# Performance work log

Measured on AMD Instinct MI355X. Metric: run time of the kernel, lower is better.

The kernel has to match this reference:

```python
import jax, jax.numpy as jnp
import numpy as np

H = 16  # num_heads (from init_kwargs)


def setup_inputs() -> dict:
    key = jax.random.key(0)
    ks = jax.random.split(key, 12)
    B, S, E = 4, 1024, 1024
    inp = {
        "query": jax.random.normal(ks[0], (B, S, E), jnp.float32),
        "key": jax.random.normal(ks[1], (B, S, E), jnp.float32),
        "value": jax.random.normal(ks[2], (B, S, E), jnp.float32),
        "mask": jax.random.randint(ks[3], (B, S, S), 0, 2, jnp.int32),
        # nn.Linear params: y = x @ W.T + b
        "Wq": jax.random.normal(ks[4], (E, E), jnp.float32) * 0.02,
        "bq": jnp.zeros((E,), jnp.float32),
        "Wk": jax.random.normal(ks[5], (E, E), jnp.float32) * 0.02,
        "bk": jnp.zeros((E,), jnp.float32),
        "Wv": jax.random.normal(ks[6], (E, E), jnp.float32) * 0.02,
        "bv": jnp.zeros((E,), jnp.float32),
        "Wo": jax.random.normal(ks[7], (E, E), jnp.float32) * 0.02,
        "bo": jnp.zeros((E,), jnp.float32),
    }
    return inp


def reference(query, key, value, mask, Wq, bq, Wk, bk, Wv, bv, Wo, bo):
    # Dropout treated as identity (eval mode) for a deterministic baseline.
    B, Sq, E = query.shape
    Sk = key.shape[1]
    D = E // H
    scale = jnp.sqrt(jnp.float32(D))

    Q = (query @ Wq.T + bq).reshape(B, Sq, H, D).transpose(0, 2, 1, 3)  # bhqd
    K = (key @ Wk.T + bk).reshape(B, Sk, H, D).transpose(0, 2, 1, 3)    # bhkd
    V = (value @ Wv.T + bv).reshape(B, Sk, H, D).transpose(0, 2, 1, 3)  # bhkd

    scores = jnp.einsum("bhqd,bhkd->bhqk", Q, K) / scale
    scores = jnp.where(mask[:, None, :, :] == 0, jnp.float32(-1e9), scores)
    attn = jax.nn.softmax(scores, axis=-1)  # [B,H,Sq,Sk]

    ctx = jnp.einsum("bhqk,bhkd->bhqd", attn, V)
    ctx = ctx.transpose(0, 2, 1, 3).reshape(B, Sq, E)
    out = ctx @ Wo.T + bo
    attn_avg = attn.mean(axis=1)  # [B,Sq,Sk]
    return out, attn_avg
```

## Files before the change

kernel.cpp:

```cpp
#include <hip/hip_runtime.h>
#include <hip/hip_bf16.h>
#include <stdint.h>

#define BATCH 4
#define SEQ   1024
#define EMB   1024
#define NH    16
#define HD    64

typedef short s8v __attribute__((ext_vector_type(8)));
typedef float f4v __attribute__((ext_vector_type(4)));

__device__ __forceinline__ uint16_t f2bf(float f) {
    __hip_bfloat16 h = __float2bfloat16(f);
    return *reinterpret_cast<uint16_t*>(&h);
}
__device__ __forceinline__ short bfraw(float f) {
    __hip_bfloat16 h = __float2bfloat16(f);
    return *reinterpret_cast<short*>(&h);
}
__device__ __forceinline__ s8v cvt8(const float* p) {
    float4 a = *(const float4*)p;
    float4 b = *(const float4*)(p + 4);
    s8v r;
    r[0] = bfraw(a.x); r[1] = bfraw(a.y); r[2] = bfraw(a.z); r[3] = bfraw(a.w);
    r[4] = bfraw(b.x); r[5] = bfraw(b.y); r[6] = bfraw(b.z); r[7] = bfraw(b.w);
    return r;
}

__global__ __launch_bounds__(256) void pack_mask(
        const int* __restrict__ mask, unsigned long long* __restrict__ Mb64)
{
    const size_t gid = (size_t)blockIdx.x * 256 + threadIdx.x;
    const unsigned long long bal = __ballot(mask[gid] != 0);
    if ((threadIdx.x & 63) == 0) Mb64[gid >> 6] = bal;
}

__global__ __launch_bounds__(256) void cvt_all(
        const float* __restrict__ W0, const float* __restrict__ W1,
        const float* __restrict__ W2, const float* __restrict__ W3,
        const float* __restrict__ X0, const float* __restrict__ X1,
        const float* __restrict__ X2,
        uint16_t* __restrict__ Wdst, uint16_t* __restrict__ Xq,
        uint16_t* __restrict__ Xk, uint16_t* __restrict__ Xv)
{
    const int y = blockIdx.y;
    const size_t off = ((size_t)blockIdx.x * 256 + threadIdx.x) * 8;
    if (y < 4) {
        if (blockIdx.x >= 512) return;
        const float* s = (y == 0) ? W0 : (y == 1) ? W1 : (y == 2) ? W2 : W3;
        *(s8v*)(Wdst + (size_t)y * EMB * EMB + off) = cvt8(s + off);
    } else {
        const float* s = (y == 4) ? X0 : (y == 5) ? X1 : X2;
        uint16_t*    d = (y == 4) ? Xq : (y == 5) ? Xk : Xv;
        *(s8v*)(d + off) = cvt8(s + off);
    }
}

__global__ __launch_bounds__(512, 2) void proj_gemm(
        const uint16_t* __restrict__ Xb, const uint16_t* __restrict__ Wb,
        const float* __restrict__ bias, void* __restrict__ outv,
        int scatter, float scale)
{
    __shared__ __attribute__((aligned(16))) uint16_t As[128][32];
    __shared__ __attribute__((aligned(16))) uint16_t Bs[128][32];

    const int t    = threadIdx.x;
    const int lane = t & 63;
    const int w    = t >> 6;
    const int wm = w & 1;
    const int wn = w >> 1;
    const int m0 = blockIdx.y * 128;
    const int n0 = blockIdx.x * 128;
    const int ar = lane & 15;
    const int aq = lane >> 4;

    const int srow = t >> 2;
    const int scol = (t & 3) * 8;

    const uint16_t* gA = Xb + (size_t)(m0 + srow) * EMB + scol;
    const uint16_t* gB = Wb + (size_t)(n0 + srow) * EMB + scol;

    f4v acc[4][2];
    #pragma unroll
    for (int i = 0; i < 4; ++i)
        #pragma unroll
        for (int j = 0; j < 2; ++j) acc[i][j] = (f4v){0.f, 0.f, 0.f, 0.f};

    s8v ra = *(const s8v*)gA;
    s8v rb = *(const s8v*)gB;

    for (int k0 = 0; k0 < EMB; k0 += 32) {
        __syncthreads();
        *(s8v*)&As[srow][scol] = ra;
        *(s8v*)&Bs[srow][scol] = rb;
        const int kn = (k0 + 32) & (EMB - 1);
        ra = *(const s8v*)(gA + kn);
        rb = *(const s8v*)(gB + kn);
        __syncthreads();

        s8v af[4], bf[2];
        #pragma unroll
        for (int i = 0; i < 4; ++i)
            af[i] = *(const s8v*)&As[wm * 64 + i * 16 + ar][aq * 8];
        #pragma unroll
        for (int j = 0; j < 2; ++j)
            bf[j] = *(const s8v*)&Bs[wn * 32 + j * 16 + ar][aq * 8];
        #pragma unroll
        for (int i = 0; i < 4; ++i)
            #pragma unroll
            for (int j = 0; j < 2; ++j)
                acc[i][j] = __builtin_amdgcn_mfma_f32_16x16x32_bf16(af[i], bf[j], acc[i][j], 0, 0, 0);
    }

    #pragma unroll
    for (int i = 0; i < 4; ++i) {
        const int crow = m0 + wm * 64 + i * 16 + aq * 4;
        #pragma unroll
        for (int j = 0; j < 2; ++j) {
            const int n = n0 + wn * 32 + j * 16 + ar;
            const float bv = bias[n];
            #pragma unroll
            for (int r = 0; r < 4; ++r) {
                const int m = crow + r;
                const float v = (acc[i][j][r] + bv) * scale;
                if (scatter == 1) {
                    size_t idx = (size_t)(((m >> 10) * NH + (n >> 6)) * SEQ + (m & 1023)) * HD + (n & 63);
                    ((uint16_t*)outv)[idx] = f2bf(v);
                } else if (scatter == 2) {
                    size_t idx = (size_t)(((m >> 10) * NH + (n >> 6)) * HD + (n & 63)) * SEQ + (m & 1023);
                    ((uint16_t*)outv)[idx] = f2bf(v);
                } else {
                    ((float*)outv)[(size_t)m * EMB + n] = v;
                }
            }
        }
    }
}

__global__ __launch_bounds__(256, 4) void flash_ctx(
        const uint16_t* __restrict__ Qb, const uint16_t* __restrict__ Kb,
        const uint16_t* __restrict__ Vt, const uint32_t* __restrict__ Mb,
        uint16_t* __restrict__ ctx, float* __restrict__ linv_out)
{
    __shared__ uint32_t Ml[4][16][33];
    __shared__ __attribute__((aligned(16))) uint16_t Pt[4][2][16][56];

    const int t = threadIdx.x;
    const int w = t >> 6, lane = t & 63;
    const int ar = lane & 15, aq = lane >> 4;

    const int id   = blockIdx.x;
    const int xcd  = id & 7;
    const int rest = id >> 3;
    const int bh   = xcd * 8 + (rest & 7);
    const int qt   = (rest >> 3) * 4 + w;
    const int b = bh >> 4, h = bh & 15;
    const size_t hb = ((size_t)(b * NH + h)) * SEQ * HD;

    {
        const uint32_t* src = Mb + (((size_t)b * SEQ + qt * 16) << 5);
        uint4 m0 = *(const uint4*)(src + lane * 8);
        uint4 m1 = *(const uint4*)(src + lane * 8 + 4);
        const int pr = (lane * 8) >> 5, pc = (lane * 8) & 31;
        Ml[w][pr][pc + 0] = m0.x; Ml[w][pr][pc + 1] = m0.y;
        Ml[w][pr][pc + 2] = m0.z; Ml[w][pr][pc + 3] = m0.w;
        Ml[w][pr][pc + 4] = m1.x; Ml[w][pr][pc + 5] = m1.y;
        Ml[w][pr][pc + 6] = m1.z; Ml[w][pr][pc + 7] = m1.w;
    }

    const uint16_t* qp = Qb + hb + (size_t)(qt * 16 + ar) * HD + aq * 8;
    const s8v a0 = *(const s8v*)qp;
    const s8v a1 = *(const s8v*)(qp + 32);

    const uint16_t* kbase = Kb + hb + (size_t)ar * HD + aq * 8;
    const uint16_t* vbase = Vt + hb + (size_t)ar * SEQ + aq * 8;

    f4v O0 = {0.f,0.f,0.f,0.f}, O1 = O0, O2 = O0, O3 = O0;
    float lsum[4] = {0.f, 0.f, 0.f, 0.f};

    s8v cbl0 = *(const s8v*)kbase;
    s8v cbh0 = *(const s8v*)(kbase + 32);
    s8v cbl1 = *(const s8v*)(kbase + 16 * HD);
    s8v cbh1 = *(const s8v*)(kbase + 16 * HD + 32);
    s8v cvv0 = *(const s8v*)vbase;
    s8v cvv1 = *(const s8v*)(vbase + 16 * SEQ);
    s8v cvv2 = *(const s8v*)(vbase + 32 * SEQ);
    s8v cvv3 = *(const s8v*)(vbase + 48 * SEQ);

    #pragma unroll 2
    for (int ci = 0; ci < 32; ++ci) {
        f4v z = {0.f,0.f,0.f,0.f};
        f4v s0 = __builtin_amdgcn_mfma_f32_16x16x32_bf16(a0, cbl0, z, 0, 0, 0);
        s0 = __builtin_amdgcn_mfma_f32_16x16x32_bf16(a1, cbh0, s0, 0, 0, 0);
        f4v s1 = __builtin_amdgcn_mfma_f32_16x16x32_bf16(a0, cbl1, z, 0, 0, 0);
        s1 = __builtin_amdgcn_mfma_f32_16x16x32_bf16(a1, cbh1, s1, 0, 0, 0);

        const int kcn = ((ci + 1) & 31) * 32;
        const uint16_t* kn = kbase + (size_t)kcn * HD;
        const uint16_t* vn = vbase + kcn;
        s8v nbl0 = *(const s8v*)kn;
        s8v nbh0 = *(const s8v*)(kn + 32);
        s8v nbl1 = *(const s8v*)(kn + 16 * HD);
        s8v nbh1 = *(const s8v*)(kn + 16 * HD + 32);
        s8v nvv0 = *(const s8v*)vn;
        s8v nvv1 = *(const s8v*)(vn + 16 * SEQ);
        s8v nvv2 = *(const s8v*)(vn + 32 * SEQ);
        s8v nvv3 = *(const s8v*)(vn + 48 * SEQ);

        const int pb = ci & 1;
        #pragma unroll
        for (int r = 0; r < 4; ++r) {
            const uint32_t mw = Ml[w][aq * 4 + r][ci];
            const float e0 = ((mw >> ar) & 1u)        ? __expf(s0[r]) : 0.f;
            const float e1 = ((mw >> (16 + ar)) & 1u) ? __expf(s1[r]) : 0.f;
            lsum[r] += e0 + e1;
            Pt[w][pb][aq * 4 + r][ar]      = f2bf(e0);
            Pt[w][pb][aq * 4 + r][16 + ar] = f2bf(e1);
        }

        const s8v pa = *(const s8v*)&Pt[w][pb][ar][aq * 8];
        O0 = __builtin_amdgcn_mfma_f32_16x16x32_bf16(pa, cvv0, O0, 0, 0, 0);
        O1 = __builtin_amdgcn_mfma_f32_16x16x32_bf16(pa, cvv1, O1, 0, 0, 0);
        O2 = __builtin_amdgcn_mfma_f32_16x16x32_bf16(pa, cvv2, O2, 0, 0, 0);
        O3 = __builtin_amdgcn_mfma_f32_16x16x32_bf16(pa, cvv3, O3, 0, 0, 0);

        cbl0 = nbl0; cbh0 = nbh0; cbl1 = nbl1; cbh1 = nbh1;
        cvv0 = nvv0; cvv1 = nvv1; cvv2 = nvv2; cvv3 = nvv3;
    }

    #pragma unroll
    for (int off = 1; off < 16; off <<= 1) {
        #pragma unroll
        for (int r = 0; r < 4; ++r) lsum[r] += __shfl_xor(lsum[r], off);
    }
    float inv[4];
    #pragma unroll
    for (int r = 0; r < 4; ++r) inv[r] = 1.0f / lsum[r];

    #pragma unroll
    for (int r = 0; r < 4; ++r) {
        const int q = qt * 16 + aq * 4 + r;
        uint16_t* cp = ctx + ((size_t)(b * SEQ + q) * NH + h) * HD + ar;
        cp[ 0] = f2bf(O0[r] * inv[r]);
        cp[16] = f2bf(O1[r] * inv[r]);
        cp[32] = f2bf(O2[r] * inv[r]);
        cp[48] = f2bf(O3[r] * inv[r]);
    }
    if (ar == 0) {
        #pragma unroll
        for (int r = 0; r < 4; ++r)
            linv_out[(size_t)(b * NH + h) * SEQ + qt * 16 + aq * 4 + r] = inv[r];
    }
}

__global__ __launch_bounds__(512, 2) void attn_avg(
        const uint16_t* __restrict__ Qb, const uint16_t* __restrict__ Kb,
        const uint32_t* __restrict__ Mb, const float* __restrict__ linv,
        float* __restrict__ attn_out)
{
    const int qt = blockIdx.x;
    const int b  = blockIdx.y >> 1;
    const int kh = blockIdx.y & 1;
    const int t = threadIdx.x;
    const int w = t >> 6, lane = t & 63;
    const int ar = lane & 15, aq = lane >> 4;
    const int k0 = kh * 512 + w * 64;

    uint32_t mw0[4], mw1[4];
    #pragma unroll
    for (int r = 0; r < 4; ++r) {
        const uint32_t* mp = Mb + (((size_t)b * SEQ + qt * 16 + aq * 4 + r) << 5) + (k0 >> 5);
        mw0[r] = mp[0]; mw1[r] = mp[1];
    }

    float acc[16];
    #pragma unroll
    for (int j = 0; j < 16; ++j) acc[j] = 0.f;

    for (int h = 0; h < NH; ++h) {
        const size_t hb = ((size_t)(b * NH + h)) * SEQ * HD;
        const uint16_t* qp = Qb + hb + (size_t)(qt * 16 + ar) * HD + aq * 8;
        const s8v a0 = *(const s8v*)qp;
        const s8v a1 = *(const s8v*)(qp + 32);
        float fs[4];
        #pragma unroll
        for (int r = 0; r < 4; ++r)
            fs[r] = linv[(size_t)(b * NH + h) * SEQ + qt * 16 + aq * 4 + r] * 0.0625f;

        #pragma unroll
        for (int nt = 0; nt < 4; ++nt) {
            const uint16_t* kp = Kb + hb + (size_t)(k0 + nt * 16 + ar) * HD + aq * 8;
            s8v bl = *(const s8v*)kp, bh2 = *(const s8v*)(kp + 32);
            f4v z = {0.f,0.f,0.f,0.f};
            f4v s = __builtin_amdgcn_mfma_f32_16x16x32_bf16(a0, bl, z, 0, 0, 0);
            s = __builtin_amdgcn_mfma_f32_16x16x32_bf16(a1, bh2, s, 0, 0, 0);
            #pragma unroll
            for (int r = 0; r < 4; ++r) {
                const uint32_t mword = (nt & 2) ? mw1[r] : mw0[r];
                const int bit = ((nt & 1) << 4) + ar;
                if ((mword >> bit) & 1u) acc[r * 4 + nt] += __expf(s[r]) * fs[r];
            }
        }
    }

    #pragma unroll
    for (int r = 0; r < 4; ++r) {
        float* ap = attn_out + ((size_t)b * SEQ + qt * 16 + aq * 4 + r) * SEQ + k0 + ar;
        #pragma unroll
        for (int nt = 0; nt < 4; ++nt) ap[nt * 16] = acc[r * 4 + nt];
    }
}

extern "C" void kernel_launch(void* const* d_in, const int* in_sizes, int n_in,
                              void* d_out, int out_size, void* d_ws, size_t ws_size,
                              hipStream_t stream) {
    const float* q_in = (const float*)d_in[0];
    const float* k_in = (const float*)d_in[1];
    const float* v_in = (const float*)d_in[2];
    const int*   mask = (const int*)d_in[3];
    const float* Wq = (const float*)d_in[4];
    const float* bq = (const float*)d_in[5];
    const float* Wk = (const float*)d_in[6];
    const float* bk = (const float*)d_in[7];
    const float* Wv = (const float*)d_in[8];
    const float* bv = (const float*)d_in[9];
    const float* Wo = (const float*)d_in[10];
    const float* bo = (const float*)d_in[11];

    float* out      = (float*)d_out;
    float* attn_out = out + (size_t)BATCH * SEQ * EMB;

    const size_t qkv_elems = (size_t)BATCH * NH * SEQ * HD;
    uint16_t* Qb  = (uint16_t*)d_ws;
    uint16_t* Kb  = Qb + qkv_elems;
    uint16_t* Vt  = Kb + qkv_elems;
    uint16_t* ctx = Vt + qkv_elems;
    uint16_t* Wcb = ctx + (size_t)BATCH * SEQ * EMB;
    uint16_t* Wqb = Wcb;
    uint16_t* Wkb = Wcb + (size_t)EMB * EMB;
    uint16_t* Wvb = Wcb + 2 * (size_t)EMB * EMB;
    uint16_t* Wob = Wcb + 3 * (size_t)EMB * EMB;
    uint16_t* Xq  = Wcb + 4 * (size_t)EMB * EMB;
    uint16_t* Xk  = Xq + qkv_elems;
    uint16_t* Xv  = ctx;
    uint32_t* Mb32 = (uint32_t*)(Xk + qkv_elems);
    float*    linv = (float*)(Mb32 + (size_t)BATCH * SEQ * 32);

    pack_mask<<<dim3((BATCH * SEQ * SEQ) / 256), 256, 0, stream>>>(
        mask, (unsigned long long*)Mb32);
    cvt_all<<<dim3(2048, 7), 256, 0, stream>>>(Wq, Wk, Wv, Wo, q_in, k_in, v_in,
                                               Wcb, Xq, Xk, Xv);

    dim3 ggrid(EMB / 128, (BATCH * SEQ) / 128);
    proj_gemm<<<ggrid, 512, 0, stream>>>(Xq, Wqb, bq, Qb, 1, 0.125f);
    proj_gemm<<<ggrid, 512, 0, stream>>>(Xk, Wkb, bk, Kb, 1, 1.0f);
    proj_gemm<<<ggrid, 512, 0, stream>>>(Xv, Wvb, bv, Vt, 2, 1.0f);

    flash_ctx<<<dim3(1024), 256, 0, stream>>>(Qb, Kb, Vt, Mb32, ctx, linv);
    attn_avg<<<dim3(SEQ / 16, BATCH * 2), 512, 0, stream>>>(Qb, Kb, Mb32, linv, attn_out);

    proj_gemm<<<ggrid, 512, 0, stream>>>(ctx, Wob, bo, out, 0, 1.0f);
}
```

Measured before the change: 411.8 us.

## Batch QKV GEMMs into one launch, split flash keys across warps, shrink tiles

The three projection GEMMs become a single launch that picks Q, K or V by blockIdx.z, and the GEMM tile drops from 128x128 with 512 threads to 64x64 with 256 threads. The flash attention kernel now splits the key range between two warp pairs and merges their partial O and row sums through shared memory, which doubles the grid. It also drops the register prefetch of the next K/V chunk. attn_avg is split into four key quarters for more blocks. The aim is fewer launches and more parallelism and occupancy, at the cost of less data reuse per tile, an extra reduction step, and less latency hiding in the flash loop.

```diff
diff --git a/kernel.cpp b/kernel.cpp
--- a/kernel.cpp
+++ b/kernel.cpp
@@ -57,21 +57,32 @@
     }
 }
 
-__global__ __launch_bounds__(512, 2) void proj_gemm(
-        const uint16_t* __restrict__ Xb, const uint16_t* __restrict__ Wb,
-        const float* __restrict__ bias, void* __restrict__ outv,
-        int scatter, float scale)
-{
-    __shared__ __attribute__((aligned(16))) uint16_t As[128][32];
-    __shared__ __attribute__((aligned(16))) uint16_t Bs[128][32];
+__global__ __launch_bounds__(256, 4) void gemm3(
+        const uint16_t* __restrict__ X0, const uint16_t* __restrict__ W0,
+        const float* __restrict__ b0, void* __restrict__ o0, int sc0, float ss0,
+        const uint16_t* __restrict__ X1, const uint16_t* __restrict__ W1,
+        const float* __restrict__ b1, void* __restrict__ o1, int sc1, float ss1,
+        const uint16_t* __restrict__ X2, const uint16_t* __restrict__ W2,
+        const float* __restrict__ b2, void* __restrict__ o2, int sc2, float ss2)
+{
+    __shared__ __attribute__((aligned(16))) uint16_t As[64][40];
+    __shared__ __attribute__((aligned(16))) uint16_t Bs[64][40];
+
+    const int z = blockIdx.z;
+    const uint16_t* Xb   = (z == 0) ? X0 : (z == 1) ? X1 : X2;
+    const uint16_t* Wb   = (z == 0) ? W0 : (z == 1) ? W1 : W2;
+    const float*    bias = (z == 0) ? b0 : (z == 1) ? b1 : b2;
+    void*           outv = (z == 0) ? o0 : (z == 1) ? o1 : o2;
+    const int     scatter = (z == 0) ? sc0 : (z == 1) ? sc1 : sc2;
+    const float   scale   = (z == 0) ? ss0 : (z == 1) ? ss1 : ss2;
 
     const int t    = threadIdx.x;
     const int lane = t & 63;
     const int w    = t >> 6;
     const int wm = w & 1;
     const int wn = w >> 1;
-    const int m0 = blockIdx.y * 128;
-    const int n0 = blockIdx.x * 128;
+    const int m0 = blockIdx.y * 64;
+    const int n0 = blockIdx.x * 64;
     const int ar = lane & 15;
     const int aq = lane >> 4;
 
@@ -81,9 +92,9 @@
     const uint16_t* gA = Xb + (size_t)(m0 + srow) * EMB + scol;
     const uint16_t* gB = Wb + (size_t)(n0 + srow) * EMB + scol;
 
-    f4v acc[4][2];
-    #pragma unroll
-    for (int i = 0; i < 4; ++i)
+    f4v acc[2][2];
+    #pragma unroll
+    for (int i = 0; i < 2; ++i)
         #pragma unroll
         for (int j = 0; j < 2; ++j) acc[i][j] = (f4v){0.f, 0.f, 0.f, 0.f};
 
@@ -99,23 +110,23 @@
         rb = *(const s8v*)(gB + kn);
         __syncthreads();
 
-        s8v af[4], bf[2];
-        #pragma unroll
-        for (int i = 0; i < 4; ++i)
-            af[i] = *(const s8v*)&As[wm * 64 + i * 16 + ar][aq * 8];
+        s8v af[2], bf[2];
+        #pragma unroll
+        for (int i = 0; i < 2; ++i)
+            af[i] = *(const s8v*)&As[wm * 32 + i * 16 + ar][aq * 8];
         #pragma unroll
         for (int j = 0; j < 2; ++j)
             bf[j] = *(const s8v*)&Bs[wn * 32 + j * 16 + ar][aq * 8];
         #pragma unroll
-        for (int i = 0; i < 4; ++i)
+        for (int i = 0; i < 2; ++i)
             #pragma unroll
             for (int j = 0; j < 2; ++j)
                 acc[i][j] = __builtin_amdgcn_mfma_f32_16x16x32_bf16(af[i], bf[j], acc[i][j], 0, 0, 0);
     }
 
     #pragma unroll
-    for (int i = 0; i < 4; ++i) {
-        const int crow = m0 + wm * 64 + i * 16 + aq * 4;
+    for (int i = 0; i < 2; ++i) {
+        const int crow = m0 + wm * 32 + i * 16 + aq * 4;
         #pragma unroll
         for (int j = 0; j < 2; ++j) {
             const int n = n0 + wn * 32 + j * 16 + ar;
@@ -138,36 +149,40 @@
     }
 }
 
-__global__ __launch_bounds__(256, 4) void flash_ctx(
+__global__ __launch_bounds__(256, 8) void flash_ctx(
         const uint16_t* __restrict__ Qb, const uint16_t* __restrict__ Kb,
         const uint16_t* __restrict__ Vt, const uint32_t* __restrict__ Mb,
         uint16_t* __restrict__ ctx, float* __restrict__ linv_out)
 {
-    __shared__ uint32_t Ml[4][16][33];
-    __shared__ __attribute__((aligned(16))) uint16_t Pt[4][2][16][56];
+    __shared__ uint32_t Ml[2][16][33];
+    __shared__ __attribute__((aligned(16))) char shbuf[14336];
+    auto Pt = reinterpret_cast<uint16_t(*)[2][16][56]>(shbuf);
+    auto Oc = reinterpret_cast<float(*)[64][21]>(shbuf);
 
     const int t = threadIdx.x;
     const int w = t >> 6, lane = t & 63;
     const int ar = lane & 15, aq = lane >> 4;
-
-    const int id   = blockIdx.x;
-    const int xcd  = id & 7;
-    const int rest = id >> 3;
-    const int bh   = xcd * 8 + (rest & 7);
-    const int qt   = (rest >> 3) * 4 + w;
+    const int qt_local = w & 1, khalf = w >> 1;
+
+    const int id    = blockIdx.x;
+    const int xcd   = id & 7;
+    const int rest  = id >> 3;
+    const int bh    = xcd * 8 + (rest & 7);
+    const int qpair = rest >> 3;
+    const int qt    = qpair * 2 + qt_local;
     const int b = bh >> 4, h = bh & 15;
     const size_t hb = ((size_t)(b * NH + h)) * SEQ * HD;
 
     {
-        const uint32_t* src = Mb + (((size_t)b * SEQ + qt * 16) << 5);
-        uint4 m0 = *(const uint4*)(src + lane * 8);
-        uint4 m1 = *(const uint4*)(src + lane * 8 + 4);
-        const int pr = (lane * 8) >> 5, pc = (lane * 8) & 31;
-        Ml[w][pr][pc + 0] = m0.x; Ml[w][pr][pc + 1] = m0.y;
-        Ml[w][pr][pc + 2] = m0.z; Ml[w][pr][pc + 3] = m0.w;
-        Ml[w][pr][pc + 4] = m1.x; Ml[w][pr][pc + 5] = m1.y;
-        Ml[w][pr][pc + 6] = m1.z; Ml[w][pr][pc + 7] = m1.w;
-    }
+        const uint32_t* src = Mb + (((size_t)b * SEQ + qpair * 32) << 5);
+        uint4 m = *(const uint4*)(src + t * 4);
+        const int row = t >> 3, col = (t & 7) * 4;
+        Ml[row >> 4][row & 15][col + 0] = m.x;
+        Ml[row >> 4][row & 15][col + 1] = m.y;
+        Ml[row >> 4][row & 15][col + 2] = m.z;
+        Ml[row >> 4][row & 15][col + 3] = m.w;
+    }
+    __syncthreads();
 
     const uint16_t* qp = Qb + hb + (size_t)(qt * 16 + ar) * HD + aq * 8;
     const s8v a0 = *(const s8v*)qp;
@@ -179,39 +194,24 @@
     f4v O0 = {0.f,0.f,0.f,0.f}, O1 = O0, O2 = O0, O3 = O0;
     float lsum[4] = {0.f, 0.f, 0.f, 0.f};
 
-    s8v cbl0 = *(const s8v*)kbase;
-    s8v cbh0 = *(const s8v*)(kbase + 32);
-    s8v cbl1 = *(const s8v*)(kbase + 16 * HD);
-    s8v cbh1 = *(const s8v*)(kbase + 16 * HD + 32);
-    s8v cvv0 = *(const s8v*)vbase;
-    s8v cvv1 = *(const s8v*)(vbase + 16 * SEQ);
-    s8v cvv2 = *(const s8v*)(vbase + 32 * SEQ);
-    s8v cvv3 = *(const s8v*)(vbase + 48 * SEQ);
-
     #pragma unroll 2
-    for (int ci = 0; ci < 32; ++ci) {
+    for (int ci = 0; ci < 16; ++ci) {
+        const int c  = khalf * 16 + ci;
+        const int kc = c * 32;
+        const uint16_t* k0 = kbase + (size_t)kc * HD;
+        const uint16_t* k1 = k0 + 16 * HD;
+        s8v bl0 = *(const s8v*)k0, bh0 = *(const s8v*)(k0 + 32);
+        s8v bl1 = *(const s8v*)k1, bh1 = *(const s8v*)(k1 + 32);
         f4v z = {0.f,0.f,0.f,0.f};
-        f4v s0 = __builtin_amdgcn_mfma_f32_16x16x32_bf16(a0, cbl0, z, 0, 0, 0);
-        s0 = __builtin_amdgcn_mfma_f32_16x16x32_bf16(a1, cbh0, s0, 0, 0, 0);
-        f4v s1 = __builtin_amdgcn_mfma_f32_16x16x32_bf16(a0, cbl1, z, 0, 0, 0);
-        s1 = __builtin_amdgcn_mfma_f32_16x16x32_bf16(a1, cbh1, s1, 0, 0, 0);
-
-        const int kcn = ((ci + 1) & 31) * 32;
-        const uint16_t* kn = kbase + (size_t)kcn * HD;
-        const uint16_t* vn = vbase + kcn;
-        s8v nbl0 = *(const s8v*)kn;
-        s8v nbh0 = *(const s8v*)(kn + 32);
-        s8v nbl1 = *(const s8v*)(kn + 16 * HD);
-        s8v nbh1 = *(const s8v*)(kn + 16 * HD + 32);
-        s8v nvv0 = *(const s8v*)vn;
-        s8v nvv1 = *(const s8v*)(vn + 16 * SEQ);
-        s8v nvv2 = *(const s8v*)(vn + 32 * SEQ);
-        s8v nvv3 = *(const s8v*)(vn + 48 * SEQ);
+        f4v s0 = __builtin_amdgcn_mfma_f32_16x16x32_bf16(a0, bl0, z, 0, 0, 0);
+        s0 = __builtin_amdgcn_mfma_f32_16x16x32_bf16(a1, bh0, s0, 0, 0, 0);
+        f4v s1 = __builtin_amdgcn_mfma_f32_16x16x32_bf16(a0, bl1, z, 0, 0, 0);
+        s1 = __builtin_amdgcn_mfma_f32_16x16x32_bf16(a1, bh1, s1, 0, 0, 0);
 
         const int pb = ci & 1;
         #pragma unroll
         for (int r = 0; r < 4; ++r) {
-            const uint32_t mw = Ml[w][aq * 4 + r][ci];
+            const uint32_t mw = Ml[qt_local][aq * 4 + r][c];
             const float e0 = ((mw >> ar) & 1u)        ? __expf(s0[r]) : 0.f;
             const float e1 = ((mw >> (16 + ar)) & 1u) ? __expf(s1[r]) : 0.f;
             lsum[r] += e0 + e1;
@@ -220,13 +220,15 @@
         }
 
         const s8v pa = *(const s8v*)&Pt[w][pb][ar][aq * 8];
-        O0 = __builtin_amdgcn_mfma_f32_16x16x32_bf16(pa, cvv0, O0, 0, 0, 0);
-        O1 = __builtin_amdgcn_mfma_f32_16x16x32_bf16(pa, cvv1, O1, 0, 0, 0);
-        O2 = __builtin_amdgcn_mfma_f32_16x16x32_bf16(pa, cvv2, O2, 0, 0, 0);
-        O3 = __builtin_amdgcn_mfma_f32_16x16x32_bf16(pa, cvv3, O3, 0, 0, 0);
-
-        cbl0 = nbl0; cbh0 = nbh0; cbl1 = nbl1; cbh1 = nbh1;
-        cvv0 = nvv0; cvv1 = nvv1; cvv2 = nvv2; cvv3 = nvv3;
+        const uint16_t* v0 = vbase + kc;
+        s8v vv0 = *(const s8v*)(v0);
+        s8v vv1 = *(const s8v*)(v0 + 16 * SEQ);
+        s8v vv2 = *(const s8v*)(v0 + 32 * SEQ);
+        s8v vv3 = *(const s8v*)(v0 + 48 * SEQ);
+        O0 = __builtin_amdgcn_mfma_f32_16x16x32_bf16(pa, vv0, O0, 0, 0, 0);
+        O1 = __builtin_amdgcn_mfma_f32_16x16x32_bf16(pa, vv1, O1, 0, 0, 0);
+        O2 = __builtin_amdgcn_mfma_f32_16x16x32_bf16(pa, vv2, O2, 0, 0, 0);
+        O3 = __builtin_amdgcn_mfma_f32_16x16x32_bf16(pa, vv3, O3, 0, 0, 0);
     }
 
     #pragma unroll
@@ -234,49 +236,68 @@
         #pragma unroll
         for (int r = 0; r < 4; ++r) lsum[r] += __shfl_xor(lsum[r], off);
     }
-    float inv[4];
-    #pragma unroll
-    for (int r = 0; r < 4; ++r) inv[r] = 1.0f / lsum[r];
-
-    #pragma unroll
-    for (int r = 0; r < 4; ++r) {
-        const int q = qt * 16 + aq * 4 + r;
-        uint16_t* cp = ctx + ((size_t)(b * SEQ + q) * NH + h) * HD + ar;
-        cp[ 0] = f2bf(O0[r] * inv[r]);
-        cp[16] = f2bf(O1[r] * inv[r]);
-        cp[32] = f2bf(O2[r] * inv[r]);
-        cp[48] = f2bf(O3[r] * inv[r]);
-    }
-    if (ar == 0) {
-        #pragma unroll
-        for (int r = 0; r < 4; ++r)
-            linv_out[(size_t)(b * NH + h) * SEQ + qt * 16 + aq * 4 + r] = inv[r];
-    }
-}
-
-__global__ __launch_bounds__(512, 2) void attn_avg(
+
+    __syncthreads();
+    if (khalf == 1) {
+        float* d = Oc[qt_local][lane];
+        #pragma unroll
+        for (int r = 0; r < 4; ++r) {
+            d[r]      = O0[r];  d[4 + r]  = O1[r];
+            d[8 + r]  = O2[r];  d[12 + r] = O3[r];
+            d[16 + r] = lsum[r];
+        }
+    }
+    __syncthreads();
+    if (khalf == 0) {
+        const float* s = Oc[qt_local][lane];
+        #pragma unroll
+        for (int r = 0; r < 4; ++r) {
+            O0[r] += s[r];      O1[r] += s[4 + r];
+            O2[r] += s[8 + r];  O3[r] += s[12 + r];
+            lsum[r] += s[16 + r];
+        }
+        float inv[4];
+        #pragma unroll
+        for (int r = 0; r < 4; ++r) inv[r] = 1.0f / lsum[r];
+
+        #pragma unroll
+        for (int r = 0; r < 4; ++r) {
+            const int q = qt * 16 + aq * 4 + r;
+            uint16_t* cp = ctx + ((size_t)(b * SEQ + q) * NH + h) * HD + ar;
+            cp[ 0] = f2bf(O0[r] * inv[r]);
+            cp[16] = f2bf(O1[r] * inv[r]);
+            cp[32] = f2bf(O2[r] * inv[r]);
+            cp[48] = f2bf(O3[r] * inv[r]);
+        }
+        if (ar == 0) {
+            #pragma unroll
+            for (int r = 0; r < 4; ++r)
+                linv_out[(size_t)(b * NH + h) * SEQ + qt * 16 + aq * 4 + r] = inv[r];
+        }
+    }
+}
+
+__global__ __launch_bounds__(512, 8) void attn_avg(
         const uint16_t* __restrict__ Qb, const uint16_t* __restrict__ Kb,
         const uint32_t* __restrict__ Mb, const float* __restrict__ linv,
         float* __restrict__ attn_out)
 {
     const int qt = blockIdx.x;
-    const int b  = blockIdx.y >> 1;
-    const int kh = blockIdx.y & 1;
+    const int b  = blockIdx.y >> 2;
+    const int kq = blockIdx.y & 3;
     const int t = threadIdx.x;
     const int w = t >> 6, lane = t & 63;
     const int ar = lane & 15, aq = lane >> 4;
-    const int k0 = kh * 512 + w * 64;
-
-    uint32_t mw0[4], mw1[4];
-    #pragma unroll
-    for (int r = 0; r < 4; ++r) {
-        const uint32_t* mp = Mb + (((size_t)b * SEQ + qt * 16 + aq * 4 + r) << 5) + (k0 >> 5);
-        mw0[r] = mp[0]; mw1[r] = mp[1];
-    }
-
-    float acc[16];
-    #pragma unroll
-    for (int j = 0; j < 16; ++j) acc[j] = 0.f;
+    const int k0 = kq * 256 + w * 32;
+
+    uint32_t mw[4];
+    #pragma unroll
+    for (int r = 0; r < 4; ++r)
+        mw[r] = Mb[(((size_t)b * SEQ + qt * 16 + aq * 4 + r) << 5) + (k0 >> 5)];
+
+    float acc[8];
+    #pragma unroll
+    for (int j = 0; j < 8; ++j) acc[j] = 0.f;
 
     for (int h = 0; h < NH; ++h) {
         const size_t hb = ((size_t)(b * NH + h)) * SEQ * HD;
@@ -289,7 +310,7 @@
             fs[r] = linv[(size_t)(b * NH + h) * SEQ + qt * 16 + aq * 4 + r] * 0.0625f;
 
         #pragma unroll
-        for (int nt = 0; nt < 4; ++nt) {
+        for (int nt = 0; nt < 2; ++nt) {
             const uint16_t* kp = Kb + hb + (size_t)(k0 + nt * 16 + ar) * HD + aq * 8;
             s8v bl = *(const s8v*)kp, bh2 = *(const s8v*)(kp + 32);
             f4v z = {0.f,0.f,0.f,0.f};
@@ -297,9 +318,8 @@
             s = __builtin_amdgcn_mfma_f32_16x16x32_bf16(a1, bh2, s, 0, 0, 0);
             #pragma unroll
             for (int r = 0; r < 4; ++r) {
-                const uint32_t mword = (nt & 2) ? mw1[r] : mw0[r];
-                const int bit = ((nt & 1) << 4) + ar;
-                if ((mword >> bit) & 1u) acc[r * 4 + nt] += __expf(s[r]) * fs[r];
+                const int bit = nt * 16 + ar;
+                if ((mw[r] >> bit) & 1u) acc[r * 2 + nt] += __expf(s[r]) * fs[r];
             }
         }
     }
@@ -308,7 +328,7 @@
     for (int r = 0; r < 4; ++r) {
         float* ap = attn_out + ((size_t)b * SEQ + qt * 16 + aq * 4 + r) * SEQ + k0 + ar;
         #pragma unroll
-        for (int nt = 0; nt < 4; ++nt) ap[nt * 16] = acc[r * 4 + nt];
+        for (int nt = 0; nt < 2; ++nt) ap[nt * 16] = acc[r * 2 + nt];
     }
 }
 
@@ -352,13 +372,18 @@
     cvt_all<<<dim3(2048, 7), 256, 0, stream>>>(Wq, Wk, Wv, Wo, q_in, k_in, v_in,
                                                Wcb, Xq, Xk, Xv);
 
-    dim3 ggrid(EMB / 128, (BATCH * SEQ) / 128);
-    proj_gemm<<<ggrid, 512, 0, stream>>>(Xq, Wqb, bq, Qb, 1, 0.125f);
-    proj_gemm<<<ggrid, 512, 0, stream>>>(Xk, Wkb, bk, Kb, 1, 1.0f);
-    proj_gemm<<<ggrid, 512, 0, stream>>>(Xv, Wvb, bv, Vt, 2, 1.0f);
-
-    flash_ctx<<<dim3(1024), 256, 0, stream>>>(Qb, Kb, Vt, Mb32, ctx, linv);
-    attn_avg<<<dim3(SEQ / 16, BATCH * 2), 512, 0, stream>>>(Qb, Kb, Mb32, linv, attn_out);
-
-    proj_gemm<<<ggrid, 512, 0, stream>>>(ctx, Wob, bo, out, 0, 1.0f);
-}
+    dim3 g3(EMB / 64, (BATCH * SEQ) / 64, 3);
+    gemm3<<<g3, 256, 0, stream>>>(
+        Xq, Wqb, bq, Qb, 1, 0.125f,
+        Xk, Wkb, bk, Kb, 1, 1.0f,
+        Xv, Wvb, bv, Vt, 2, 1.0f);
+
+    flash_ctx<<<dim3(2048), 256, 0, stream>>>(Qb, Kb, Vt, Mb32, ctx, linv);
+    attn_avg<<<dim3(SEQ / 16, BATCH * 4), 512, 0, stream>>>(Qb, Kb, Mb32, linv, attn_out);
+
+    dim3 g1(EMB / 64, (BATCH * SEQ) / 64, 1);
+    gemm3<<<g1, 256, 0, stream>>>(
+        ctx, Wob, bo, out, 0, 1.0f,
+        ctx, Wob, bo, out, 0, 1.0f,
+        ctx, Wob, bo, out, 0, 1.0f);
+}
```

Result: slower. 516.8 us (+25.5%).

## Batch QKV GEMMs, pad LDS tiles, dual-stream flash loop, split attn_avg finer

Applied to the files above, without the earlier changes.

The three Q/K/V projection GEMMs become one launch with blockIdx.z selecting the operands, and the LDS tiles get a row pad from 32 to 40 elements to cut bank conflicts. The flash_ctx loop now handles two key chunks per iteration with separate accumulators instead of software-prefetching the next chunk, which aims for more MFMA independence but needs more registers. attn_avg splits keys into quarters instead of halves with launch bounds of 4 blocks, doubling the block count and reducing per-thread state.

```diff
diff --git a/kernel.cpp b/kernel.cpp
--- a/kernel.cpp
+++ b/kernel.cpp
@@ -57,13 +57,24 @@
     }
 }
 
-__global__ __launch_bounds__(512, 2) void proj_gemm(
-        const uint16_t* __restrict__ Xb, const uint16_t* __restrict__ Wb,
-        const float* __restrict__ bias, void* __restrict__ outv,
-        int scatter, float scale)
+__global__ __launch_bounds__(512, 2) void gemm3(
+        const uint16_t* __restrict__ X0, const uint16_t* __restrict__ W0,
+        const float* __restrict__ b0, void* __restrict__ o0, int sc0, float ss0,
+        const uint16_t* __restrict__ X1, const uint16_t* __restrict__ W1,
+        const float* __restrict__ b1, void* __restrict__ o1, int sc1, float ss1,
+        const uint16_t* __restrict__ X2, const uint16_t* __restrict__ W2,
+        const float* __restrict__ b2, void* __restrict__ o2, int sc2, float ss2)
 {
-    __shared__ __attribute__((aligned(16))) uint16_t As[128][32];
-    __shared__ __attribute__((aligned(16))) uint16_t Bs[128][32];
+    __shared__ __attribute__((aligned(16))) uint16_t As[128][40];
+    __shared__ __attribute__((aligned(16))) uint16_t Bs[128][40];
+
+    const int z = blockIdx.z;
+    const uint16_t* Xb   = (z == 0) ? X0 : (z == 1) ? X1 : X2;
+    const uint16_t* Wb   = (z == 0) ? W0 : (z == 1) ? W1 : W2;
+    const float*    bias = (z == 0) ? b0 : (z == 1) ? b1 : b2;
+    void*           outv = (z == 0) ? o0 : (z == 1) ? o1 : o2;
+    const int     scatter = (z == 0) ? sc0 : (z == 1) ? sc1 : sc2;
+    const float   scale   = (z == 0) ? ss0 : (z == 1) ? ss1 : ss2;
 
     const int t    = threadIdx.x;
     const int lane = t & 63;
@@ -176,57 +187,80 @@
     const uint16_t* kbase = Kb + hb + (size_t)ar * HD + aq * 8;
     const uint16_t* vbase = Vt + hb + (size_t)ar * SEQ + aq * 8;
 
-    f4v O0 = {0.f,0.f,0.f,0.f}, O1 = O0, O2 = O0, O3 = O0;
-    float lsum[4] = {0.f, 0.f, 0.f, 0.f};
-
-    s8v cbl0 = *(const s8v*)kbase;
-    s8v cbh0 = *(const s8v*)(kbase + 32);
-    s8v cbl1 = *(const s8v*)(kbase + 16 * HD);
-    s8v cbh1 = *(const s8v*)(kbase + 16 * HD + 32);
-    s8v cvv0 = *(const s8v*)vbase;
-    s8v cvv1 = *(const s8v*)(vbase + 16 * SEQ);
-    s8v cvv2 = *(const s8v*)(vbase + 32 * SEQ);
-    s8v cvv3 = *(const s8v*)(vbase + 48 * SEQ);
-
-    #pragma unroll 2
-    for (int ci = 0; ci < 32; ++ci) {
+    f4v OA0 = {0.f,0.f,0.f,0.f}, OA1 = OA0, OA2 = OA0, OA3 = OA0;
+    f4v OB0 = OA0, OB1 = OA0, OB2 = OA0, OB3 = OA0;
+    float lsA[4] = {0.f, 0.f, 0.f, 0.f};
+    float lsB[4] = {0.f, 0.f, 0.f, 0.f};
+
+    for (int ci = 0; ci < 16; ++ci) {
+        const int cA = ci * 2, cB = ci * 2 + 1;
+        const int kcA = cA * 32, kcB = cB * 32;
+
+        const uint16_t* kA = kbase + (size_t)kcA * HD;
+        const uint16_t* kB = kbase + (size_t)kcB * HD;
+        s8v Abl0 = *(const s8v*)kA,            Abh0 = *(const s8v*)(kA + 32);
+        s8v Abl1 = *(const s8v*)(kA + 16*HD),  Abh1 = *(const s8v*)(kA + 16*HD + 32);
+        s8v Bbl0 = *(const s8v*)kB,            Bbh0 = *(const s8v*)(kB + 32);
+        s8v Bbl1 = *(const s8v*)(kB + 16*HD),  Bbh1 = *(const s8v*)(kB + 16*HD + 32);
+
         f4v z = {0.f,0.f,0.f,0.f};
-        f4v s0 = __builtin_amdgcn_mfma_f32_16x16x32_bf16(a0, cbl0, z, 0, 0, 0);
-        s0 = __builtin_amdgcn_mfma_f32_16x16x32_bf16(a1, cbh0, s0, 0, 0, 0);
-        f4v s1 = __builtin_amdgcn_mfma_f32_16x16x32_bf16(a0, cbl1, z, 0, 0, 0);
-        s1 = __builtin_amdgcn_mfma_f32_16x16x32_bf16(a1, cbh1, s1, 0, 0, 0);
-
-        const int kcn = ((ci + 1) & 31) * 32;
-        const uint16_t* kn = kbase + (size_t)kcn * HD;
-        const uint16_t* vn = vbase + kcn;
-        s8v nbl0 = *(const s8v*)kn;
-        s8v nbh0 = *(const s8v*)(kn + 32);
-        s8v nbl1 = *(const s8v*)(kn + 16 * HD);
-        s8v nbh1 = *(const s8v*)(kn + 16 * HD + 32);
-        s8v nvv0 = *(const s8v*)vn;
-        s8v nvv1 = *(const s8v*)(vn + 16 * SEQ);
-        s8v nvv2 = *(const s8v*)(vn + 32 * SEQ);
-        s8v nvv3 = *(const s8v*)(vn + 48 * SEQ);
-
-        const int pb = ci & 1;
+        f4v sA0 = __builtin_amdgcn_mfma_f32_16x16x32_bf16(a0, Abl0, z, 0, 0, 0);
+        sA0 = __builtin_amdgcn_mfma_f32_16x16x32_bf16(a1, Abh0, sA0, 0, 0, 0);
+        f4v sA1 = __builtin_amdgcn_mfma_f32_16x16x32_bf16(a0, Abl1, z, 0, 0, 0);
+        sA1 = __builtin_amdgcn_mfma_f32_16x16x32_bf16(a1, Abh1, sA1, 0, 0, 0);
+        f4v sB0 = __builtin_amdgcn_mfma_f32_16x16x32_bf16(a0, Bbl0, z, 0, 0, 0);
+        sB0 = __builtin_amdgcn_mfma_f32_16x16x32_bf16(a1, Bbh0, sB0, 0, 0, 0);
+        f4v sB1 = __builtin_amdgcn_mfma_f32_16x16x32_bf16(a0, Bbl1, z, 0, 0, 0);
+        sB1 = __builtin_amdgcn_mfma_f32_16x16x32_bf16(a1, Bbh1, sB1, 0, 0, 0);
+
+        const uint16_t* vA = vbase + kcA;
+        const uint16_t* vB = vbase + kcB;
+        s8v Av0 = *(const s8v*)(vA);
+        s8v Av1 = *(const s8v*)(vA + 16 * SEQ);
+        s8v Av2 = *(const s8v*)(vA + 32 * SEQ);
+        s8v Av3 = *(const s8v*)(vA + 48 * SEQ);
+        s8v Bv0 = *(const s8v*)(vB);
+        s8v Bv1 = *(const s8v*)(vB + 16 * SEQ);
+        s8v Bv2 = *(const s8v*)(vB + 32 * SEQ);
+        s8v Bv3 = *(const s8v*)(vB + 48 * SEQ);
+
         #pragma unroll
         for (int r = 0; r < 4; ++r) {
-            const uint32_t mw = Ml[w][aq * 4 + r][ci];
-            const float e0 = ((mw >> ar) & 1u)        ? __expf(s0[r]) : 0.f;
-            const float e1 = ((mw >> (16 + ar)) & 1u) ? __expf(s1[r]) : 0.f;
-            lsum[r] += e0 + e1;
-            Pt[w][pb][aq * 4 + r][ar]      = f2bf(e0);
-            Pt[w][pb][aq * 4 + r][16 + ar] = f2bf(e1);
+            const uint32_t mwA = Ml[w][aq * 4 + r][cA];
+            const float e0 = ((mwA >> ar) & 1u)        ? __expf(sA0[r]) : 0.f;
+            const float e1 = ((mwA >> (16 + ar)) & 1u) ? __expf(sA1[r]) : 0.f;
+            lsA[r] += e0 + e1;
+            Pt[w][0][aq * 4 + r][ar]      = f2bf(e0);
+            Pt[w][0][aq * 4 + r][16 + ar] = f2bf(e1);
         }
-
-        const s8v pa = *(const s8v*)&Pt[w][pb][ar][aq * 8];
-        O0 = __builtin_amdgcn_mfma_f32_16x16x32_bf16(pa, cvv0, O0, 0, 0, 0);
-        O1 = __builtin_amdgcn_mfma_f32_16x16x32_bf16(pa, cvv1, O1, 0, 0, 0);
-        O2 = __builtin_amdgcn_mfma_f32_16x16x32_bf16(pa, cvv2, O2, 0, 0, 0);
-        O3 = __builtin_amdgcn_mfma_f32_16x16x32_bf16(pa, cvv3, O3, 0, 0, 0);
-
-        cbl0 = nbl0; cbh0 = nbh0; cbl1 = nbl1; cbh1 = nbh1;
-        cvv0 = nvv0; cvv1 = nvv1; cvv2 = nvv2; cvv3 = nvv3;
+        #pragma unroll
+        for (int r = 0; r < 4; ++r) {
+            const uint32_t mwB = Ml[w][aq * 4 + r][cB];
+            const float e0 = ((mwB >> ar) & 1u)        ? __expf(sB0[r]) : 0.f;
+            const float e1 = ((mwB >> (16 + ar)) & 1u) ? __expf(sB1[r]) : 0.f;
+            lsB[r] += e0 + e1;
+            Pt[w][1][aq * 4 + r][ar]      = f2bf(e0);
+            Pt[w][1][aq * 4 + r][16 + ar] = f2bf(e1);
+        }
+
+        const s8v paA = *(const s8v*)&Pt[w][0][ar][aq * 8];
+        OA0 = __builtin_amdgcn_mfma_f32_16x16x32_bf16(paA, Av0, OA0, 0, 0, 0);
+        OA1 = __builtin_amdgcn_mfma_f32_16x16x32_bf16(paA, Av1, OA1, 0, 0, 0);
+        OA2 = __builtin_amdgcn_mfma_f32_16x16x32_bf16(paA, Av2, OA2, 0, 0, 0);
+        OA3 = __builtin_amdgcn_mfma_f32_16x16x32_bf16(paA, Av3, OA3, 0, 0, 0);
+        const s8v paB = *(const s8v*)&Pt[w][1][ar][aq * 8];
+        OB0 = __builtin_amdgcn_mfma_f32_16x16x32_bf16(paB, Bv0, OB0, 0, 0, 0);
+        OB1 = __builtin_amdgcn_mfma_f32_16x16x32_bf16(paB, Bv1, OB1, 0, 0, 0);
+        OB2 = __builtin_amdgcn_mfma_f32_16x16x32_bf16(paB, Bv2, OB2, 0, 0, 0);
+        OB3 = __builtin_amdgcn_mfma_f32_16x16x32_bf16(paB, Bv3, OB3, 0, 0, 0);
+    }
+
+    float lsum[4];
+    #pragma unroll
+    for (int r = 0; r < 4; ++r) {
+        OA0[r] += OB0[r]; OA1[r] += OB1[r];
+        OA2[r] += OB2[r]; OA3[r] += OB3[r];
+        lsum[r] = lsA[r] + lsB[r];
     }
 
     #pragma unroll
@@ -242,10 +276,10 @@
     for (int r = 0; r < 4; ++r) {
         const int q = qt * 16 + aq * 4 + r;
         uint16_t* cp = ctx + ((size_t)(b * SEQ + q) * NH + h) * HD + ar;
-        cp[ 0] = f2bf(O0[r] * inv[r]);
-        cp[16] = f2bf(O1[r] * inv[r]);
-        cp[32] = f2bf(O2[r] * inv[r]);
-        cp[48] = f2bf(O3[r] * inv[r]);
+        cp[ 0] = f2bf(OA0[r] * inv[r]);
+        cp[16] = f2bf(OA1[r] * inv[r]);
+        cp[32] = f2bf(OA2[r] * inv[r]);
+        cp[48] = f2bf(OA3[r] * inv[r]);
     }
     if (ar == 0) {
         #pragma unroll
@@ -254,29 +288,27 @@
     }
 }
 
-__global__ __launch_bounds__(512, 2) void attn_avg(
+__global__ __launch_bounds__(512, 4) void attn_avg(
         const uint16_t* __restrict__ Qb, const uint16_t* __restrict__ Kb,
         const uint32_t* __restrict__ Mb, const float* __restrict__ linv,
         float* __restrict__ attn_out)
 {
     const int qt = blockIdx.x;
-    const int b  = blockIdx.y >> 1;
-    const int kh = blockIdx.y & 1;
+    const int b  = blockIdx.y >> 2;
+    const int kq = blockIdx.y & 3;
     const int t = threadIdx.x;
     const int w = t >> 6, lane = t & 63;
     const int ar = lane & 15, aq = lane >> 4;
-    const int k0 = kh * 512 + w * 64;
-
-    uint32_t mw0[4], mw1[4];
-    #pragma unroll
-    for (int r = 0; r < 4; ++r) {
-        const uint32_t* mp = Mb + (((size_t)b * SEQ + qt * 16 + aq * 4 + r) << 5) + (k0 >> 5);
-        mw0[r] = mp[0]; mw1[r] = mp[1];
-    }
-
-    float acc[16];
-    #pragma unroll
-    for (int j = 0; j < 16; ++j) acc[j] = 0.f;
+    const int k0 = kq * 256 + w * 32;
+
+    uint32_t mw[4];
+    #pragma unroll
+    for (int r = 0; r < 4; ++r)
+        mw[r] = Mb[(((size_t)b * SEQ + qt * 16 + aq * 4 + r) << 5) + (k0 >> 5)];
+
+    float acc[8];
+    #pragma unroll
+    for (int j = 0; j < 8; ++j) acc[j] = 0.f;
 
     for (int h = 0; h < NH; ++h) {
         const size_t hb = ((size_t)(b * NH + h)) * SEQ * HD;
@@ -289,7 +321,7 @@
             fs[r] = linv[(size_t)(b * NH + h) * SEQ + qt * 16 + aq * 4 + r] * 0.0625f;
 
         #pragma unroll
-        for (int nt = 0; nt < 4; ++nt) {
+        for (int nt = 0; nt < 2; ++nt) {
             const uint16_t* kp = Kb + hb + (size_t)(k0 + nt * 16 + ar) * HD + aq * 8;
             s8v bl = *(const s8v*)kp, bh2 = *(const s8v*)(kp + 32);
             f4v z = {0.f,0.f,0.f,0.f};
@@ -297,9 +329,8 @@
             s = __builtin_amdgcn_mfma_f32_16x16x32_bf16(a1, bh2, s, 0, 0, 0);
             #pragma unroll
             for (int r = 0; r < 4; ++r) {
-                const uint32_t mword = (nt & 2) ? mw1[r] : mw0[r];
-                const int bit = ((nt & 1) << 4) + ar;
-                if ((mword >> bit) & 1u) acc[r * 4 + nt] += __expf(s[r]) * fs[r];
+                const int bit = nt * 16 + ar;
+                if ((mw[r] >> bit) & 1u) acc[r * 2 + nt] += __expf(s[r]) * fs[r];
             }
         }
     }
@@ -308,7 +339,7 @@
     for (int r = 0; r < 4; ++r) {
         float* ap = attn_out + ((size_t)b * SEQ + qt * 16 + aq * 4 + r) * SEQ + k0 + ar;
         #pragma unroll
-        for (int nt = 0; nt < 4; ++nt) ap[nt * 16] = acc[r * 4 + nt];
+        for (int nt = 0; nt < 2; ++nt) ap[nt * 16] = acc[r * 2 + nt];
     }
 }
 
@@ -352,13 +383,18 @@
     cvt_all<<<dim3(2048, 7), 256, 0, stream>>>(Wq, Wk, Wv, Wo, q_in, k_in, v_in,
                                                Wcb, Xq, Xk, Xv);
 
-    dim3 ggrid(EMB / 128, (BATCH * SEQ) / 128);
-    proj_gemm<<<ggrid, 512, 0, stream>>>(Xq, Wqb, bq, Qb, 1, 0.125f);
-    proj_gemm<<<ggrid, 512, 0, stream>>>(Xk, Wkb, bk, Kb, 1, 1.0f);
-    proj_gemm<<<ggrid, 512, 0, stream>>>(Xv, Wvb, bv, Vt, 2, 1.0f);
+    dim3 g3(EMB / 128, (BATCH * SEQ) / 128, 3);
+    gemm3<<<g3, 512, 0, stream>>>(
+        Xq, Wqb, bq, Qb, 1, 0.125f,
+        Xk, Wkb, bk, Kb, 1, 1.0f,
+        Xv, Wvb, bv, Vt, 2, 1.0f);
 
     flash_ctx<<<dim3(1024), 256, 0, stream>>>(Qb, Kb, Vt, Mb32, ctx, linv);
-    attn_avg<<<dim3(SEQ / 16, BATCH * 2), 512, 0, stream>>>(Qb, Kb, Mb32, linv, attn_out);
-
-    proj_gemm<<<ggrid, 512, 0, stream>>>(ctx, Wob, bo, out, 0, 1.0f);
-}
+    attn_avg<<<dim3(SEQ / 16, BATCH * 4), 512, 0, stream>>>(Qb, Kb, Mb32, linv, attn_out);
+
+    dim3 g1(EMB / 128, (BATCH * SEQ) / 128, 1);
+    gemm3<<<g1, 512, 0, stream>>>(
+        ctx, Wob, bo, out, 0, 1.0f,
+        ctx, Wob, bo, out, 0, 1.0f,
+        ctx, Wob, bo, out, 0, 1.0f);
+}
```

Measured after the change: 408.6 us. No clear change (-0.8%).
